# Performance work log

Hardware: AMD Instinct MI355X
Metric: run time of the kernel (lower is better)

The kernel has to match this reference:

```python
import jax, jax.numpy as jnp
import numpy as np

N, E = 50000, 800000
IN = OUT = 128
T, R, H = 4, 6, 8
DK = OUT // H


def setup_inputs() -> dict:
    key = jax.random.key(0)
    ks = iter(jax.random.split(key, 24))
    nk = lambda: next(ks)
    return {
        "node_inp": jax.random.normal(nk(), (N, IN), jnp.float32),
        "node_type": jax.random.randint(nk(), (N,), 0, T),
        "edge_index": jax.random.randint(nk(), (2, E), 0, N),
        "edge_type": jax.random.randint(nk(), (E,), 0, R),
        "edge_sign": jax.random.randint(nk(), (E,), -2, 2),
        "edge_distance": jax.random.uniform(nk(), (E,), jnp.float32, 0.0, 2e5),
        "Wq": jax.random.normal(nk(), (T, IN, OUT), jnp.float32) / np.float32(np.sqrt(IN)),
        "bq": jnp.zeros((T, OUT), jnp.float32),
        "Wk": jax.random.normal(nk(), (T, IN, OUT), jnp.float32) / np.float32(np.sqrt(IN)),
        "bk": jnp.zeros((T, OUT), jnp.float32),
        "Wv": jax.random.normal(nk(), (T, IN, OUT), jnp.float32) / np.float32(np.sqrt(IN)),
        "bv": jnp.zeros((T, OUT), jnp.float32),
        "rel_q": jax.random.normal(nk(), (R, H, DK), jnp.float32) * 0.2,
        "rel_k": jax.random.normal(nk(), (R, H, DK), jnp.float32) * 0.2,
        "rel_v": jax.random.normal(nk(), (R, H, DK), jnp.float32) * 0.2,
        "sign_k_neutral": jnp.ones((H, DK), jnp.float32),
        "sign_v_neutral": jnp.ones((H, DK), jnp.float32),
        "rel_bias": jnp.zeros((R, H), jnp.float32),
        "dist_alpha": jnp.asarray(0.5, jnp.float32),
        "dist_tau": jnp.asarray(100000.0, jnp.float32),
        "skip": jnp.ones((T,), jnp.float32),
        "ln_gamma": jnp.ones((T, OUT), jnp.float32),
        "ln_beta": jnp.zeros((T, OUT), jnp.float32),
    }


def reference(node_inp, node_type, edge_index, edge_type, edge_sign, edge_distance,
              Wq, bq, Wk, bk, Wv, bv, rel_q, rel_k, rel_v,
              sign_k_neutral, sign_v_neutral, rel_bias, dist_alpha, dist_tau,
              skip, ln_gamma, ln_beta):
    n = node_inp.shape[0]
    src, dst = edge_index[0], edge_index[1]

    # edge_sign normalization: anything < -1 or == 0 -> -2 (neutral), else clamp to {-1, 1}
    es = jnp.where((edge_sign < -1) | (edge_sign == 0), -2, jnp.clip(edge_sign, -1, 1))
    sign_idx = jnp.where(es == -1, 0, jnp.where(es == 1, 1, 2))  # [E]

    # per-type Q/K/V projections, then select by node_type
    idx = jnp.arange(n)
    Q = (jnp.einsum('ni,tio->tno', node_inp, Wq) + bq[:, None, :])[node_type, idx]
    K = (jnp.einsum('ni,tio->tno', node_inp, Wk) + bk[:, None, :])[node_type, idx]
    V = (jnp.einsum('ni,tio->tno', node_inp, Wv) + bv[:, None, :])[node_type, idx]
    Q = Q.reshape(n, H, DK); K = K.reshape(n, H, DK); V = V.reshape(n, H, DK)

    sign_k_all = jnp.concatenate([-jnp.ones((1, H, DK), Q.dtype), jnp.ones((1, H, DK), Q.dtype), sign_k_neutral[None]], 0)
    sign_v_all = jnp.concatenate([-jnp.ones((1, H, DK), Q.dtype), jnp.ones((1, H, DK), Q.dtype), sign_v_neutral[None]], 0)

    q_eff = Q[dst] * rel_q[edge_type]                        # [E,H,DK]
    k_eff = K[src] * rel_k[edge_type] * sign_k_all[sign_idx]  # [E,H,DK]
    v_eff = V[src] * rel_v[edge_type] * sign_v_all[sign_idx]  # [E,H,DK]

    scores = (q_eff * k_eff).sum(-1) / np.float32(np.sqrt(DK))  # [E,H]
    scores = scores + rel_bias[edge_type]
    phi = dist_alpha * jnp.exp(-edge_distance / (dist_tau + 1e-9))
    scores = scores + phi[:, None]

    # destination-grouped softmax over edges
    m = jax.ops.segment_max(scores, dst, num_segments=n)      # [N,H]
    ex = jnp.exp(scores - m[dst])
    Z = jax.ops.segment_sum(ex, dst, num_segments=n)          # [N,H]
    attn = ex / (Z[dst] + 1e-9)                               # [E,H]

    msg = (v_eff * attn[..., None]).reshape(-1, OUT)          # [E,OUT]
    out = jax.ops.segment_sum(msg, dst, num_segments=n)       # [N,OUT]

    alpha = jax.nn.sigmoid(skip)[node_type][:, None]          # [N,1]
    mix = alpha * out + (1.0 - alpha) * node_inp
    mu = mix.mean(-1, keepdims=True)
    var = ((mix - mu) ** 2).mean(-1, keepdims=True)
    normed = (mix - mu) / jnp.sqrt(var + 1e-5)
    return normed * ln_gamma[node_type] + ln_beta[node_type]
```

## Files before the change

### kernel.cpp

```cpp
#include <hip/hip_runtime.h>

#define N_NODES 50000
#define N_EDGES 800000
#define DIM 128
#define NT 4
#define NR 6
#define NH 8
#define NBLK_SCAN ((N_NODES + 255) / 256)
#define NBLK2 ((N_NODES + 1023) / 1024)
#define NTILE_ROW 3129
#define NPAD_MAX (NTILE_ROW * 16)

#define XCVT_N (N_NODES * DIM / 4)
#define WT_N   (NT * 3 * DIM * DIM)
#define WCB_N  (24 * 32)
#define PREP_TOTAL (XCVT_N + WT_N + WCB_N)
#define PREP_BLOCKS ((PREP_TOTAL + 255) / 256)
#define HIST_BLOCKS (N_EDGES / 256)
#define A_PREP_BASE NBLK_SCAN
#define A_HIST_BASE (NBLK_SCAN + PREP_BLOCKS)
#define A_BLOCKS (A_HIST_BASE + HIST_BLOCKS)

typedef __attribute__((ext_vector_type(8))) short bf16x8;
typedef __attribute__((ext_vector_type(4))) float f32x4;

__device__ __forceinline__ unsigned short f2bf(float f) {
    unsigned int u = __float_as_uint(f);
    return (unsigned short)((u + 0x7fffu + ((u >> 16) & 1u)) >> 16);
}
__device__ __forceinline__ float blo(unsigned int u) { return __uint_as_float(u << 16); }
__device__ __forceinline__ float bhi(unsigned int u) { return __uint_as_float(u & 0xffff0000u); }

__device__ __forceinline__ int sign_index(int s) {
    if (s < -1 || s == 0) return 2;
    return (s == -1) ? 0 : 1;
}

__global__ __launch_bounds__(256) void k_A(
    const int* __restrict__ ntype, int* __restrict__ bhist, int* __restrict__ opad,
    const float* __restrict__ x,
    const float* __restrict__ Wq, const float* __restrict__ Wk, const float* __restrict__ Wv,
    const float* __restrict__ rel_q, const float* __restrict__ rel_k,
    const float* __restrict__ rel_v,
    const float* __restrict__ skn, const float* __restrict__ svn,
    unsigned short* __restrict__ xb, unsigned short* __restrict__ Wt,
    uint4* __restrict__ wcb,
    const int* __restrict__ ei, int* __restrict__ cnt, int* __restrict__ posw)
{
    int blk = blockIdx.x;
    if (blk < NBLK_SCAN) {
        __shared__ int h[NT];
        if (threadIdx.x < NT) h[threadIdx.x] = 0;
        __syncthreads();
        int n = blk * 256 + threadIdx.x;
        if (n < N_NODES) atomicAdd(&h[ntype[n]], 1);
        if (n < NPAD_MAX) opad[n] = -1;
        __syncthreads();
        if (threadIdx.x < NT) bhist[blk * NT + threadIdx.x] = h[threadIdx.x];
        return;
    }
    if (blk < A_HIST_BASE) {
        int i = (blk - A_PREP_BASE) * 256 + threadIdx.x;
        if (i < XCVT_N) {
            float4 v = ((const float4*)x)[i];
            ushort4 o;
            o.x = f2bf(v.x); o.y = f2bf(v.y); o.z = f2bf(v.z); o.w = f2bf(v.w);
            ((ushort4*)xb)[i] = o;
        } else if (i < XCVT_N + WT_N) {
            int j = i - XCVT_N;
            int in = j & 127;
            int b2 = j >> 7;
            int out = b2 & 127;
            int ts = b2 >> 7;
            int sel = ts % 3, t = ts / 3;
            const float* W = sel == 0 ? Wq : (sel == 1 ? Wk : Wv);
            Wt[j] = f2bf(W[((size_t)t * DIM + in) * DIM + out]);
        } else if (i < PREP_TOTAL) {
            int j = i - XCVT_N - WT_N;
            int p = j & 31;
            int cmb = j >> 5;
            int et = cmb & 7, sidx = cmb >> 3;
            if (et < NR) {
                int h2 = p >> 2;
                float wk[4], wv[4];
                #pragma unroll
                for (int q = 0; q < 4; ++q) {
                    int o = 4 * p + q;
                    int rb = (et * NH + h2) * 16 + (o & 15);
                    float sgk = sidx == 0 ? -1.f : (sidx == 1 ? 1.f : skn[o]);
                    float sgv = sidx == 0 ? -1.f : (sidx == 1 ? 1.f : svn[o]);
                    wk[q] = rel_q[rb] * rel_k[rb] * sgk * 0.25f;
                    wv[q] = rel_v[rb] * sgv;
                }
                uint4 u;
                u.x = (unsigned)f2bf(wk[0]) | ((unsigned)f2bf(wk[1]) << 16);
                u.y = (unsigned)f2bf(wv[0]) | ((unsigned)f2bf(wv[1]) << 16);
                u.z = (unsigned)f2bf(wk[2]) | ((unsigned)f2bf(wk[3]) << 16);
                u.w = (unsigned)f2bf(wv[2]) | ((unsigned)f2bf(wv[3]) << 16);
                wcb[cmb * 32 + p] = u;
            }
        }
        return;
    }
    int e = (blk - A_HIST_BASE) * 256 + threadIdx.x;
    if (e < N_EDGES) posw[e] = atomicAdd(&cnt[ei[N_EDGES + e]], 1);
}

__global__ __launch_bounds__(1024) void k_B(
    const int* __restrict__ bhist, int* __restrict__ bbase, int* __restrict__ pb_g,
    const int* __restrict__ cnt, int* __restrict__ offs, int* __restrict__ bsum)
{
    int tid = threadIdx.x;
    if (blockIdx.x == 0) {
        __shared__ int s[1024];
        __shared__ int pb[NT + 1];
        int t = tid / NBLK_SCAN;
        int b = tid - t * NBLK_SCAN;
        int v = (tid < NT * NBLK_SCAN) ? bhist[b * NT + t] : 0;
        s[tid] = v;
        __syncthreads();
        for (int d = 1; d < 1024; d <<= 1) {
            int add = (tid >= d) ? s[tid - d] : 0;
            __syncthreads();
            s[tid] += add;
            __syncthreads();
        }
        if (tid == 0) {
            int acc = 0;
            for (int tt = 0; tt < NT; ++tt) {
                pb[tt] = acc;
                int tot = s[(tt + 1) * NBLK_SCAN - 1] - (tt ? s[tt * NBLK_SCAN - 1] : 0);
                acc += ((tot + 15) >> 4) << 4;
            }
            pb[NT] = acc;
        }
        __syncthreads();
        if (tid < NT * NBLK_SCAN) {
            int excl = s[tid] - v;
            int base_t = t ? s[t * NBLK_SCAN - 1] : 0;
            bbase[b * NT + t] = pb[t] + (excl - base_t);
        }
        if (tid <= NT) pb_g[tid] = pb[tid];
        return;
    }
    int sb = blockIdx.x - 1;
    __shared__ int s[1024];
    int i = sb * 1024 + tid;
    int v = (i < N_NODES) ? cnt[i] : 0;
    s[tid] = v;
    __syncthreads();
    for (int d = 1; d < 1024; d <<= 1) {
        int add = (tid >= d) ? s[tid - d] : 0;
        __syncthreads();
        s[tid] += add;
        __syncthreads();
    }
    if (i < N_NODES) offs[i] = s[tid] - v;
    if (tid == 1023) bsum[sb] = s[1023];
}

__global__ __launch_bounds__(256) void k_C(
    const int* __restrict__ ntype, const int* __restrict__ bbase, int* __restrict__ order_pad,
    int* __restrict__ slot,
    const int* __restrict__ bsum, int* __restrict__ bofs, int* __restrict__ offs)
{
    int blk = blockIdx.x;
    if (blk < NBLK_SCAN) {
        __shared__ int cur[NT];
        if (threadIdx.x < NT) cur[threadIdx.x] = bbase[blk * NT + threadIdx.x];
        __syncthreads();
        int n = blk * 256 + threadIdx.x;
        if (n < N_NODES) {
            int t = ntype[n];
            int pos = atomicAdd(&cur[t], 1);
            order_pad[pos] = n;
            slot[n] = pos;
        }
        return;
    }
    __shared__ int s[256];
    int t = threadIdx.x;
    int v = (t < NBLK2) ? bsum[t] : 0;
    s[t] = v;
    __syncthreads();
    for (int d = 1; d < 256; d <<= 1) {
        int add = (t >= d) ? s[t - d] : 0;
        __syncthreads();
        s[t] += add;
        __syncthreads();
    }
    if (t < NBLK2) {
        int b = s[t] - v;
        bofs[t] = b;
        if (t == NBLK2 - 1) offs[N_NODES] = N_EDGES - b;
    }
}

__global__ __launch_bounds__(256) void k_D(
    const unsigned short* __restrict__ xb, const unsigned short* __restrict__ Wt,
    const int* __restrict__ order_pad, const int* __restrict__ pb_g,
    const float* __restrict__ bq, const float* __restrict__ bk, const float* __restrict__ bv,
    float* __restrict__ Qf, unsigned short* __restrict__ KVu,
    const int* __restrict__ slot,
    const int* __restrict__ ei, const int* __restrict__ etype,
    const int* __restrict__ esign, const float* __restrict__ edist,
    const float* __restrict__ dalpha, const float* __restrict__ dtau,
    const int* __restrict__ offs, const int* __restrict__ bofs,
    const int* __restrict__ posw, int2* __restrict__ edata)
{
    int b = blockIdx.x;
    if (b >= NTILE_ROW) {
        int e = (b - NTILE_ROW) * 256 + threadIdx.x;
        if (e >= N_EDGES) return;
        int dst = ei[N_EDGES + e];
        int pos = offs[dst] + bofs[dst >> 10] + posw[e];
        int cmb = sign_index(esign[e]) * 8 + etype[e];
        float phi = dalpha[0] * __expf(-edist[e] / (dtau[0] + 1e-9f));
        int sslot = slot[ei[e]];
        edata[pos] = make_int2(sslot | (cmb << 16), __float_as_int(phi));
        return;
    }
    int row0 = b * 16;
    if (row0 >= pb_g[NT]) return;
    int t = (row0 >= pb_g[3]) ? 3 : (row0 >= pb_g[2]) ? 2 : (row0 >= pb_g[1]) ? 1 : 0;
    int wave = threadIdx.x >> 6, lane = threadIdx.x & 63;
    int arow = row0 + (lane & 15);
    int nidA = order_pad[arow];
    const unsigned short* xrow = xb + (size_t)(nidA < 0 ? 0 : nidA) * DIM;
    int ko = (lane >> 4) * 8;
    bf16x8 afrag[4];
    #pragma unroll
    for (int kt = 0; kt < 4; ++kt) afrag[kt] = *(const bf16x8*)(xrow + kt * 32 + ko);

    __shared__ unsigned short kvt[16 * 256];
    #pragma unroll
    for (int g = 0; g < 6; ++g) {
        int ocol = g * 64 + wave * 16 + (lane & 15);
        int sel = ocol >> 7, wcol = ocol & 127;
        const unsigned short* wrow = Wt + ((size_t)(t * 3 + sel) * DIM + wcol) * DIM;
        f32x4 acc = {0.f, 0.f, 0.f, 0.f};
        #pragma unroll
        for (int kt = 0; kt < 4; ++kt) {
            bf16x8 bfr = *(const bf16x8*)(wrow + kt * 32 + ko);
            acc = __builtin_amdgcn_mfma_f32_16x16x32_bf16(afrag[kt], bfr, acc, 0, 0, 0);
        }
        const float* bias_p = sel == 0 ? bq : (sel == 1 ? bk : bv);
        float bias = bias_p[t * DIM + wcol];
        #pragma unroll
        for (int r = 0; r < 4; ++r) {
            int lrow = (lane >> 4) * 4 + r;
            float v = acc[r] + bias;
            if (sel == 0) Qf[(size_t)(row0 + lrow) * DIM + wcol] = v;
            else kvt[lrow * 256 + (wcol >> 1) * 4 + (wcol & 1) + (sel == 2 ? 2 : 0)] = f2bf(v);
        }
    }
    __syncthreads();
    const uint4* s4 = (const uint4*)kvt;
    uint4* d4 = (uint4*)KVu + (size_t)row0 * 32;
    d4[threadIdx.x] = s4[threadIdx.x];
    d4[256 + threadIdx.x] = s4[256 + threadIdx.x];
}

__global__ __launch_bounds__(256) void k_attn(
    const float4* __restrict__ Qf4, const uint4* __restrict__ KV,
    const uint4* __restrict__ WCB,
    const float* __restrict__ x, const int* __restrict__ ntype,
    const int* __restrict__ slot,
    const int* __restrict__ offs, const int* __restrict__ bofs,
    const int2* __restrict__ edata,
    const float* __restrict__ rbias, const float* __restrict__ skip,
    const float* __restrict__ gmm, const float* __restrict__ bta,
    float* __restrict__ out)
{
    __shared__ float rb_s[NR * NH];
    if (threadIdx.x < NR * NH) rb_s[threadIdx.x] = rbias[threadIdx.x];
    __syncthreads();
    const int wave = threadIdx.x >> 6, lane = threadIdx.x & 63;
    const int n = blockIdx.x * 4 + wave;
    const int p = lane & 31;
    const int hi = lane >> 5;
    const int h = p >> 2;
    const int beg = offs[n] + bofs[n >> 10];
    const int end = offs[n + 1] + bofs[(n + 1) >> 10];

    const int sl = slot[n];
    const float4 q4 = Qf4[(size_t)sl * 32 + p];

    float Z = 0.f, a0 = 0.f, a1 = 0.f, a2 = 0.f, a3 = 0.f;

    auto process = [&](int2 r) {
        int src = r.x & 0xffff;
        unsigned cmb = ((unsigned)r.x) >> 16;
        uint4 kv = KV[(size_t)src * 32 + p];
        uint4 w = WCB[cmb * 32 + p];
        float pp = (q4.x * blo(w.x)) * blo(kv.x);
        pp = fmaf(q4.y * bhi(w.x), bhi(kv.x), pp);
        pp = fmaf(q4.z * blo(w.z), blo(kv.z), pp);
        pp = fmaf(q4.w * bhi(w.z), bhi(kv.z), pp);
        pp += __shfl_xor(pp, 1, 4);
        pp += __shfl_xor(pp, 2, 4);
        float ex = __expf(pp + rb_s[(cmb & 7) * NH + h] + __int_as_float(r.y));
        Z += ex;
        a0 = fmaf(blo(kv.y) * blo(w.y), ex, a0);
        a1 = fmaf(bhi(kv.y) * bhi(w.y), ex, a1);
        a2 = fmaf(blo(kv.w) * blo(w.w), ex, a2);
        a3 = fmaf(bhi(kv.w) * bhi(w.w), ex, a3);
    };

    int rem = end - beg;
    int j = beg;
    if (rem >= 4) {
        int2 r0 = edata[j + hi];
        int2 r1 = edata[j + 2 + hi];
        while (true) {
            int2 c0 = r0, c1 = r1;
            j += 4; rem -= 4;
            if (rem >= 4) { r0 = edata[j + hi]; r1 = edata[j + 2 + hi]; }
            process(c0);
            process(c1);
            if (rem < 4) break;
        }
    }
    while (rem >= 2) {
        int2 c = edata[j + hi];
        process(c);
        j += 2; rem -= 2;
    }
    if (rem) {
        int2 r = edata[j];
        int src = r.x & 0xffff;
        unsigned cmb = ((unsigned)r.x) >> 16;
        uint4 kv = KV[(size_t)src * 32 + p];
        uint4 w = WCB[cmb * 32 + p];
        float pp = (q4.x * blo(w.x)) * blo(kv.x);
        pp = fmaf(q4.y * bhi(w.x), bhi(kv.x), pp);
        pp = fmaf(q4.z * blo(w.z), blo(kv.z), pp);
        pp = fmaf(q4.w * bhi(w.z), bhi(kv.z), pp);
        pp += __shfl_xor(pp, 1, 4);
        pp += __shfl_xor(pp, 2, 4);
        float ex = __expf(pp + rb_s[(cmb & 7) * NH + h] + __int_as_float(r.y));
        ex = hi ? 0.f : ex;
        Z += ex;
        a0 = fmaf(blo(kv.y) * blo(w.y), ex, a0);
        a1 = fmaf(bhi(kv.y) * bhi(w.y), ex, a1);
        a2 = fmaf(blo(kv.w) * blo(w.w), ex, a2);
        a3 = fmaf(bhi(kv.w) * bhi(w.w), ex, a3);
    }

    Z  += __shfl_xor(Z, 32, 64);
    a0 += __shfl_xor(a0, 32, 64);
    a1 += __shfl_xor(a1, 32, 64);
    a2 += __shfl_xor(a2, 32, 64);
    a3 += __shfl_xor(a3, 32, 64);

    float rz = 1.f / (Z + 1e-9f);
    int t = ntype[n];
    float alpha = 1.f / (1.f + __expf(-skip[t]));
    float4 x4 = ((const float4*)x)[(size_t)n * 32 + p];
    float m0 = fmaf(alpha, a0 * rz - x4.x, x4.x);
    float m1 = fmaf(alpha, a1 * rz - x4.y, x4.y);
    float m2 = fmaf(alpha, a2 * rz - x4.z, x4.z);
    float m3 = fmaf(alpha, a3 * rz - x4.w, x4.w);

    float s = (m0 + m1) + (m2 + m3);
    float s2 = fmaf(m0, m0, m1 * m1) + fmaf(m2, m2, m3 * m3);
    #pragma unroll
    for (int d = 32; d >= 1; d >>= 1) {
        s += __shfl_xor(s, d, 64);
        s2 += __shfl_xor(s2, d, 64);
    }
    float mu = s * (1.f / (2 * DIM));
    float var = s2 * (1.f / (2 * DIM)) - mu * mu;
    float rstd = rsqrtf(var + 1e-5f);
    if (hi == 0) {
        float4 g4 = ((const float4*)gmm)[t * 32 + p];
        float4 b4 = ((const float4*)bta)[t * 32 + p];
        float4 o4;
        o4.x = (m0 - mu) * rstd * g4.x + b4.x;
        o4.y = (m1 - mu) * rstd * g4.y + b4.y;
        o4.z = (m2 - mu) * rstd * g4.z + b4.z;
        o4.w = (m3 - mu) * rstd * g4.w + b4.w;
        ((float4*)out)[(size_t)n * 32 + p] = o4;
    }
}

extern "C" void kernel_launch(void* const* d_in, const int* in_sizes, int n_in,
                              void* d_out, int out_size, void* d_ws, size_t ws_size,
                              hipStream_t stream) {
    const float* x      = (const float*)d_in[0];
    const int*   ntype  = (const int*)d_in[1];
    const int*   ei     = (const int*)d_in[2];
    const int*   etype  = (const int*)d_in[3];
    const int*   esign  = (const int*)d_in[4];
    const float* edist  = (const float*)d_in[5];
    const float* Wq     = (const float*)d_in[6];
    const float* bq     = (const float*)d_in[7];
    const float* Wk     = (const float*)d_in[8];
    const float* bk     = (const float*)d_in[9];
    const float* Wv     = (const float*)d_in[10];
    const float* bv     = (const float*)d_in[11];
    const float* rel_q  = (const float*)d_in[12];
    const float* rel_k  = (const float*)d_in[13];
    const float* rel_v  = (const float*)d_in[14];
    const float* skn    = (const float*)d_in[15];
    const float* svn    = (const float*)d_in[16];
    const float* rbias  = (const float*)d_in[17];
    const float* dalpha = (const float*)d_in[18];
    const float* dtau   = (const float*)d_in[19];
    const float* skip   = (const float*)d_in[20];
    const float* gmm    = (const float*)d_in[21];
    const float* bta    = (const float*)d_in[22];
    float* out = (float*)d_out;

    char* ws = (char*)d_ws;
    float*          Qf     = (float*)         (ws + 0);
    unsigned short* KVu    = (unsigned short*)(ws + 25700000);
    unsigned short* xb     = (unsigned short*)(ws + 51400000);
    unsigned short* Wt     = (unsigned short*)(ws + 64200000);
    uint4*          wcb    = (uint4*)         (ws + 64600000);
    int*            cnt    = (int*)           (ws + 64700000);
    int*            offs   = (int*)           (ws + 64900000);
    int*            bsum   = (int*)           (ws + 65200000);
    int*            bofs   = (int*)           (ws + 65210000);
    int*            posw   = (int*)           (ws + 65300000);
    int2*           edata  = (int2*)          (ws + 68600000);
    int*            opad   = (int*)           (ws + 75000000);
    int*            slot   = (int*)           (ws + 75220000);
    int*            bhist  = (int*)           (ws + 75450000);
    int*            bbase  = (int*)           (ws + 75460000);
    int*            pb     = (int*)           (ws + 75470000);

    hipMemsetAsync(cnt, 0, (size_t)N_NODES * 4, stream);
    k_A <<<A_BLOCKS, 256, 0, stream>>>(ntype, bhist, opad,
                                       x, Wq, Wk, Wv, rel_q, rel_k, rel_v, skn, svn,
                                       xb, Wt, wcb, ei, cnt, posw);
    k_B <<<1 + NBLK2, 1024, 0, stream>>>(bhist, bbase, pb, cnt, offs, bsum);
    k_C <<<NBLK_SCAN + 1, 256, 0, stream>>>(ntype, bbase, opad, slot, bsum, bofs, offs);
    k_D <<<NTILE_ROW + HIST_BLOCKS, 256, 0, stream>>>(xb, Wt, opad, pb, bq, bk, bv,
                                                      Qf, KVu, slot,
                                                      ei, etype, esign, edist, dalpha, dtau,
                                                      offs, bofs, posw, edata);
    k_attn <<<N_NODES / 4, 256, 0, stream>>>((const float4*)Qf, (const uint4*)KVu,
                                             (const uint4*)wcb, x, ntype, slot, offs, bofs,
                                             edata, rbias, skip, gmm, bta, out);
}
```

Measured before the change: 185.8 us.

## Interleave K/V per column and drop LDS staging in projection kernel

Changes the packed K/V layout so each 32-bit word holds the K and V bf16 values of the same output column, with the relation weight table repacked to match. The projection kernel now computes K and V together with paired MFMA accumulators and writes packed words straight to global memory, removing the shared-memory tile and its barrier. Workspace offsets are realigned to page-friendly boundaries. The attention inner loop is updated to read the new pairing. The direct global stores are 4-byte scattered writes rather than 16-byte coalesced copies, which may cost write efficiency.

```diff
diff --git a/kernel.cpp b/kernel.cpp
--- a/kernel.cpp
+++ b/kernel.cpp
@@ -82,21 +82,18 @@
             int et = cmb & 7, sidx = cmb >> 3;
             if (et < NR) {
                 int h2 = p >> 2;
-                float wk[4], wv[4];
+                unsigned d[4];
                 #pragma unroll
                 for (int q = 0; q < 4; ++q) {
                     int o = 4 * p + q;
                     int rb = (et * NH + h2) * 16 + (o & 15);
                     float sgk = sidx == 0 ? -1.f : (sidx == 1 ? 1.f : skn[o]);
                     float sgv = sidx == 0 ? -1.f : (sidx == 1 ? 1.f : svn[o]);
-                    wk[q] = rel_q[rb] * rel_k[rb] * sgk * 0.25f;
-                    wv[q] = rel_v[rb] * sgv;
+                    float wk = rel_q[rb] * rel_k[rb] * sgk * 0.25f;
+                    float wv = rel_v[rb] * sgv;
+                    d[q] = (unsigned)f2bf(wk) | ((unsigned)f2bf(wv) << 16);
                 }
-                uint4 u;
-                u.x = (unsigned)f2bf(wk[0]) | ((unsigned)f2bf(wk[1]) << 16);
-                u.y = (unsigned)f2bf(wv[0]) | ((unsigned)f2bf(wv[1]) << 16);
-                u.z = (unsigned)f2bf(wk[2]) | ((unsigned)f2bf(wk[3]) << 16);
-                u.w = (unsigned)f2bf(wv[2]) | ((unsigned)f2bf(wv[3]) << 16);
+                uint4 u; u.x = d[0]; u.y = d[1]; u.z = d[2]; u.w = d[3];
                 wcb[cmb * 32 + p] = u;
             }
         }
@@ -200,7 +197,7 @@
     const unsigned short* __restrict__ xb, const unsigned short* __restrict__ Wt,
     const int* __restrict__ order_pad, const int* __restrict__ pb_g,
     const float* __restrict__ bq, const float* __restrict__ bk, const float* __restrict__ bv,
-    float* __restrict__ Qf, unsigned short* __restrict__ KVu,
+    float* __restrict__ Qf, unsigned int* __restrict__ KVu,
     const int* __restrict__ slot,
     const int* __restrict__ ei, const int* __restrict__ etype,
     const int* __restrict__ esign, const float* __restrict__ edist,
@@ -224,6 +221,7 @@
     if (row0 >= pb_g[NT]) return;
     int t = (row0 >= pb_g[3]) ? 3 : (row0 >= pb_g[2]) ? 2 : (row0 >= pb_g[1]) ? 1 : 0;
     int wave = threadIdx.x >> 6, lane = threadIdx.x & 63;
+    int col = wave * 16 + (lane & 15);
     int arow = row0 + (lane & 15);
     int nidA = order_pad[arow];
     const unsigned short* xrow = xb + (size_t)(nidA < 0 ? 0 : nidA) * DIM;
@@ -232,33 +230,45 @@
     #pragma unroll
     for (int kt = 0; kt < 4; ++kt) afrag[kt] = *(const bf16x8*)(xrow + kt * 32 + ko);
 
-    __shared__ unsigned short kvt[16 * 256];
     #pragma unroll
-    for (int g = 0; g < 6; ++g) {
-        int ocol = g * 64 + wave * 16 + (lane & 15);
-        int sel = ocol >> 7, wcol = ocol & 127;
-        const unsigned short* wrow = Wt + ((size_t)(t * 3 + sel) * DIM + wcol) * DIM;
+    for (int g = 0; g < 2; ++g) {
+        int wcol = g * 64 + col;
+        const unsigned short* wrow = Wt + ((size_t)(t * 3 + 0) * DIM + wcol) * DIM;
         f32x4 acc = {0.f, 0.f, 0.f, 0.f};
         #pragma unroll
         for (int kt = 0; kt < 4; ++kt) {
             bf16x8 bfr = *(const bf16x8*)(wrow + kt * 32 + ko);
             acc = __builtin_amdgcn_mfma_f32_16x16x32_bf16(afrag[kt], bfr, acc, 0, 0, 0);
         }
-        const float* bias_p = sel == 0 ? bq : (sel == 1 ? bk : bv);
-        float bias = bias_p[t * DIM + wcol];
+        float bias = bq[t * DIM + wcol];
         #pragma unroll
         for (int r = 0; r < 4; ++r) {
             int lrow = (lane >> 4) * 4 + r;
-            float v = acc[r] + bias;
-            if (sel == 0) Qf[(size_t)(row0 + lrow) * DIM + wcol] = v;
-            else kvt[lrow * 256 + (wcol >> 1) * 4 + (wcol & 1) + (sel == 2 ? 2 : 0)] = f2bf(v);
-        }
-    }
-    __syncthreads();
-    const uint4* s4 = (const uint4*)kvt;
-    uint4* d4 = (uint4*)KVu + (size_t)row0 * 32;
-    d4[threadIdx.x] = s4[threadIdx.x];
-    d4[256 + threadIdx.x] = s4[256 + threadIdx.x];
+            Qf[(size_t)(row0 + lrow) * DIM + wcol] = acc[r] + bias;
+        }
+    }
+    #pragma unroll
+    for (int g = 0; g < 2; ++g) {
+        int wcol = g * 64 + col;
+        const unsigned short* wrowK = Wt + ((size_t)(t * 3 + 1) * DIM + wcol) * DIM;
+        const unsigned short* wrowV = Wt + ((size_t)(t * 3 + 2) * DIM + wcol) * DIM;
+        f32x4 accK = {0.f, 0.f, 0.f, 0.f};
+        f32x4 accV = {0.f, 0.f, 0.f, 0.f};
+        #pragma unroll
+        for (int kt = 0; kt < 4; ++kt) {
+            bf16x8 bK = *(const bf16x8*)(wrowK + kt * 32 + ko);
+            bf16x8 bV = *(const bf16x8*)(wrowV + kt * 32 + ko);
+            accK = __builtin_amdgcn_mfma_f32_16x16x32_bf16(afrag[kt], bK, accK, 0, 0, 0);
+            accV = __builtin_amdgcn_mfma_f32_16x16x32_bf16(afrag[kt], bV, accV, 0, 0, 0);
+        }
+        float bk_ = bk[t * DIM + wcol], bv_ = bv[t * DIM + wcol];
+        #pragma unroll
+        for (int r = 0; r < 4; ++r) {
+            int lrow = (lane >> 4) * 4 + r;
+            unsigned d = (unsigned)f2bf(accK[r] + bk_) | ((unsigned)f2bf(accV[r] + bv_) << 16);
+            KVu[(size_t)(row0 + lrow) * DIM + wcol] = d;
+        }
+    }
 }
 
 __global__ __launch_bounds__(256) void k_attn(
@@ -294,16 +304,16 @@
         uint4 kv = KV[(size_t)src * 32 + p];
         uint4 w = WCB[cmb * 32 + p];
         float pp = (q4.x * blo(w.x)) * blo(kv.x);
-        pp = fmaf(q4.y * bhi(w.x), bhi(kv.x), pp);
+        pp = fmaf(q4.y * blo(w.y), blo(kv.y), pp);
         pp = fmaf(q4.z * blo(w.z), blo(kv.z), pp);
-        pp = fmaf(q4.w * bhi(w.z), bhi(kv.z), pp);
+        pp = fmaf(q4.w * blo(w.w), blo(kv.w), pp);
         pp += __shfl_xor(pp, 1, 4);
         pp += __shfl_xor(pp, 2, 4);
         float ex = __expf(pp + rb_s[(cmb & 7) * NH + h] + __int_as_float(r.y));
         Z += ex;
-        a0 = fmaf(blo(kv.y) * blo(w.y), ex, a0);
+        a0 = fmaf(bhi(kv.x) * bhi(w.x), ex, a0);
         a1 = fmaf(bhi(kv.y) * bhi(w.y), ex, a1);
-        a2 = fmaf(blo(kv.w) * blo(w.w), ex, a2);
+        a2 = fmaf(bhi(kv.z) * bhi(w.z), ex, a2);
         a3 = fmaf(bhi(kv.w) * bhi(w.w), ex, a3);
     };
 
@@ -333,17 +343,17 @@
         uint4 kv = KV[(size_t)src * 32 + p];
         uint4 w = WCB[cmb * 32 + p];
         float pp = (q4.x * blo(w.x)) * blo(kv.x);
-        pp = fmaf(q4.y * bhi(w.x), bhi(kv.x), pp);
+        pp = fmaf(q4.y * blo(w.y), blo(kv.y), pp);
         pp = fmaf(q4.z * blo(w.z), blo(kv.z), pp);
-        pp = fmaf(q4.w * bhi(w.z), bhi(kv.z), pp);
+        pp = fmaf(q4.w * blo(w.w), blo(kv.w), pp);
         pp += __shfl_xor(pp, 1, 4);
         pp += __shfl_xor(pp, 2, 4);
         float ex = __expf(pp + rb_s[(cmb & 7) * NH + h] + __int_as_float(r.y));
         ex = hi ? 0.f : ex;
         Z += ex;
-        a0 = fmaf(blo(kv.y) * blo(w.y), ex, a0);
+        a0 = fmaf(bhi(kv.x) * bhi(w.x), ex, a0);
         a1 = fmaf(bhi(kv.y) * bhi(w.y), ex, a1);
-        a2 = fmaf(blo(kv.w) * blo(w.w), ex, a2);
+        a2 = fmaf(bhi(kv.z) * bhi(w.z), ex, a2);
         a3 = fmaf(bhi(kv.w) * bhi(w.w), ex, a3);
     }
 
@@ -414,21 +424,21 @@
 
     char* ws = (char*)d_ws;
     float*          Qf     = (float*)         (ws + 0);
-    unsigned short* KVu    = (unsigned short*)(ws + 25700000);
-    unsigned short* xb     = (unsigned short*)(ws + 51400000);
-    unsigned short* Wt     = (unsigned short*)(ws + 64200000);
-    uint4*          wcb    = (uint4*)         (ws + 64600000);
-    int*            cnt    = (int*)           (ws + 64700000);
-    int*            offs   = (int*)           (ws + 64900000);
-    int*            bsum   = (int*)           (ws + 65200000);
-    int*            bofs   = (int*)           (ws + 65210000);
-    int*            posw   = (int*)           (ws + 65300000);
-    int2*           edata  = (int2*)          (ws + 68600000);
-    int*            opad   = (int*)           (ws + 75000000);
-    int*            slot   = (int*)           (ws + 75220000);
-    int*            bhist  = (int*)           (ws + 75450000);
-    int*            bbase  = (int*)           (ws + 75460000);
-    int*            pb     = (int*)           (ws + 75470000);
+    unsigned int*   KVu    = (unsigned int*)  (ws + 25632768);
+    unsigned short* xb     = (unsigned short*)(ws + 51265536);
+    unsigned short* Wt     = (unsigned short*)(ws + 64065536);
+    uint4*          wcb    = (uint4*)         (ws + 64458752);
+    int*            cnt    = (int*)           (ws + 64471040);
+    int*            offs   = (int*)           (ws + 64672256);
+    int*            bsum   = (int*)           (ws + 64873472);
+    int*            bofs   = (int*)           (ws + 64873984);
+    int*            posw   = (int*)           (ws + 64874496);
+    int2*           edata  = (int2*)          (ws + 68074496);
+    int*            opad   = (int*)           (ws + 74475008);
+    int*            slot   = (int*)           (ws + 74675712);
+    int*            bhist  = (int*)           (ws + 74876416);
+    int*            bbase  = (int*)           (ws + 74880512);
+    int*            pb     = (int*)           (ws + 74884608);
 
     hipMemsetAsync(cnt, 0, (size_t)N_NODES * 4, stream);
     k_A <<<A_BLOCKS, 256, 0, stream>>>(ntype, bhist, opad,
```

Measured after the change: 183.7 us. Within noise of the previous version (-1.1%).
